# Kernel tuning notes

Hardware: AMD Instinct MI355X
Metric: run time of the kernel (lower is better)

The kernel has to match this reference:

```python
import jax, jax.numpy as jnp
import numpy as np

B_, L_, DIN, DM, DS, DR, K = 2, 1024, 1024, 2048, 16, 128, 4


def setup_inputs() -> dict:
    key = jax.random.key(0)
    ks = jax.random.split(key, 10)
    s = lambda k, shape, sc=0.02: (jax.random.normal(k, shape, jnp.float32) * sc)
    A_init = jnp.tile(jnp.arange(1, DS + 1, dtype=jnp.float32)[None, :], (DM, 1))  # (DM, DS)
    return {
        'x_in': jax.random.normal(ks[0], (B_, L_, DIN), jnp.float32),
        'W_in': s(ks[1], (DIN, DM)),
        'W_res': s(ks[2], (DIN, DM)),
        'W_out': s(ks[3], (DM, DIN)),
        'conv_w': s(ks[4], (DM, K), 0.1),   # depthwise conv weight (torch shape (DM,1,K) squeezed)
        'conv_b': jnp.zeros((DM,), jnp.float32),
        'A_log': jnp.log(A_init),
        'D': jnp.ones((DM,), jnp.float32),
        'W_B': s(ks[5], (DM, DS)),
        'W_C': s(ks[6], (DM, DS)),
        'W_dt': s(ks[7], (DM, DR)),
        'dt_w': s(ks[8], (DR, DM)),
        'dt_b': jnp.zeros((DM,), jnp.float32),
    }


def reference(x_in, W_in, W_res, W_out, conv_w, conv_b, A_log, D, W_B, W_C, W_dt, dt_w, dt_b):
    Bb, L, _ = x_in.shape
    x = x_in @ W_in                     # (B, L, DM)
    res = x_in @ W_res                  # (B, L, DM)
    # Causal depthwise conv1d: pad left k-1, truncate to L (matches Conv1d(padding=k-1)[:, :, :L])
    xp = jnp.pad(x, ((0, 0), (K - 1, 0), (0, 0)))
    xc = conv_b
    for i in range(K):
        xc = xc + xp[:, i:i + L, :] * conv_w[:, i]
    xc = jax.nn.silu(xc)                # (B, L, DM)
    # Selective SSM (fused_ssm)
    A = -jnp.exp(A_log)                 # (DM, DS)
    Bp = xc @ W_B                       # (B, L, DS)
    Cp = xc @ W_C                       # (B, L, DS)
    delta = jax.nn.softplus((xc @ W_dt) @ dt_w + dt_b)  # (B, L, DM)
    dA = jnp.exp(delta[..., None] * A)                       # (B, L, DM, DS)
    dBu = delta[..., None] * Bp[:, :, None, :] * xc[..., None]  # (B, L, DM, DS)

    def step(h, inp):
        dA_t, dBu_t, C_t = inp
        h = dA_t * h + dBu_t                         # (B, DM, DS)
        y = jnp.einsum('bdn,bn->bd', h, C_t)         # (B, DM)
        return h, y

    h0 = jnp.zeros((Bb, DM, DS), jnp.float32)
    _, ys = jax.lax.scan(step, h0, (dA.transpose(1, 0, 2, 3), dBu.transpose(1, 0, 2, 3), Cp.transpose(1, 0, 2)))
    y = ys.transpose(1, 0, 2) + D * xc  # (B, L, DM)
    y = y * jax.nn.silu(res)
    return y @ W_out                    # (B, L, DIN)
```

## Files before the change

kernel.cpp:

```cpp
#include <hip/hip_runtime.h>
#include <hip/hip_bf16.h>

constexpr int B_  = 2;
constexpr int L_  = 1024;
constexpr int DIN = 1024;
constexpr int DM  = 2048;
constexpr int DS  = 16;
constexpr int DR  = 128;
constexpr int KC  = 4;
constexpr int M_  = B_ * L_;
constexpr int NP2 = 256;
constexpr int KSLICES = 8;
constexpr int KSL = DM / KSLICES;
constexpr int OSLICES = 2;
constexpr int OSL = DM / OSLICES;

constexpr int NC = 32;
constexpr int CL = L_ / NC;
constexpr int S_ = B_ * DM * DS;

typedef __bf16 bf16x8 __attribute__((ext_vector_type(8)));
typedef float  f32x4  __attribute__((ext_vector_type(4)));

__device__ __forceinline__ void gload_lds16(const void* g, void* l) {
    __builtin_amdgcn_global_load_lds(
        (const __attribute__((address_space(1))) void*)g,
        (__attribute__((address_space(3))) void*)l, 16, 0, 0);
}

__device__ __forceinline__ void transpose_block(const float* __restrict__ in,
                                                __bf16* __restrict__ out,
                                                int R, int C, int bx, int by, int t) {
    __shared__ float tile[32][33];
    int tx = t & 31, ty = t >> 5;
    #pragma unroll
    for (int j = 0; j < 32; j += 8)
        tile[ty + j][tx] = in[(size_t)(by * 32 + ty + j) * C + (bx * 32 + tx)];
    __syncthreads();
    #pragma unroll
    for (int j = 0; j < 32; j += 8)
        out[(size_t)(bx * 32 + ty + j) * R + (by * 32 + tx)] = (__bf16)tile[tx][ty + j];
}

__global__ void prep_all(const float* __restrict__ x_in, const float* __restrict__ W_in,
                         const float* __restrict__ W_res, const float* __restrict__ W_out,
                         const float* __restrict__ dt_w,
                         const float* __restrict__ W_B, const float* __restrict__ W_C,
                         const float* __restrict__ W_dt,
                         __bf16* __restrict__ xinB, __bf16* __restrict__ WinT,
                         __bf16* __restrict__ WresT, __bf16* __restrict__ WoutT,
                         __bf16* __restrict__ dtwT, __bf16* __restrict__ projW) {
    int blk = blockIdx.x, t = threadIdx.x;
    if (blk < 8192) {
        int i = blk * 256 + t;
        xinB[i] = (__bf16)x_in[i];
    } else if (blk < 10240) {
        int b = blk - 8192;
        transpose_block(W_in, WinT, DIN, DM, b % 64, b / 64, t);
    } else if (blk < 12288) {
        int b = blk - 10240;
        transpose_block(W_res, WresT, DIN, DM, b % 64, b / 64, t);
    } else if (blk < 14336) {
        int b = blk - 12288;
        transpose_block(W_out, WoutT, DM, DIN, b % 32, b / 32, t);
    } else if (blk < 14592) {
        int b = blk - 14336;
        transpose_block(dt_w, dtwT, DR, DM, b % 64, b / 64, t);
    } else {
        int i = (blk - 14592) * 256 + t;
        int k = i % DM;
        int n = i / DM;
        float v = 0.f;
        if (n < 16)        v = W_B[(size_t)k * DS + n];
        else if (n < 32)   v = W_C[(size_t)k * DS + (n - 16)];
        else if (n < 160)  v = W_dt[(size_t)k * DR + (n - 32)];
        projW[i] = (__bf16)v;
    }
}

__global__ void reduce_split(const float* __restrict__ Ppart, float* __restrict__ Bp,
                             float* __restrict__ Cp, __bf16* __restrict__ dtmpB) {
    int i = blockIdx.x * 256 + threadIdx.x;
    int row = i / 160, c = i % 160;
    float v = 0.f;
    #pragma unroll
    for (int ks = 0; ks < KSLICES; ks++)
        v += Ppart[(size_t)ks * M_ * NP2 + (size_t)row * NP2 + c];
    if (c < 16)       Bp[(size_t)row * DS + c] = v;
    else if (c < 32)  Cp[(size_t)row * DS + (c - 16)] = v;
    else              dtmpB[(size_t)row * DR + (c - 32)] = (__bf16)v;
}

__global__ void reduce_out(const float* __restrict__ Opart, float* __restrict__ out) {
    int i = blockIdx.x * 256 + threadIdx.x;
    f32x4 s = ((const f32x4*)Opart)[i];
    #pragma unroll
    for (int ks = 1; ks < OSLICES; ks++)
        s += ((const f32x4*)(Opart + (size_t)ks * M_ * DIN))[i];
    ((f32x4*)out)[i] = s;
}

template<int EPI>
__global__ void gemm_tile128(const __bf16* __restrict__ A, const __bf16* __restrict__ BT,
                             float* __restrict__ Cf, __bf16* __restrict__ Cb,
                             const float* __restrict__ bias, int M, int N, int K,
                             int lda, int ldb) {
    __shared__ __bf16 sA[128 * 32];
    __shared__ __bf16 sB[128 * 32];
    int t = threadIdx.x;
    int lane = t & 63, w = t >> 6;
    int wm = w >> 1, wn = w & 1;
    int m0 = blockIdx.y * 128, n0 = blockIdx.x * 128;
    int kbase = blockIdx.z * K;
    int q = lane >> 4, rr = lane & 15;

    f32x4 acc[4][4] = {};

    int srow = t >> 2;
    int slot = t & 3;

    for (int kt = 0; kt < K; kt += 32) {
        __syncthreads();
        #pragma unroll
        for (int rnd = 0; rnd < 2; rnd++) {
            int row = srow + rnd * 64;
            int gkb = slot ^ ((row >> 1) & 3);
            const __bf16* ga = A  + (size_t)(m0 + row) * lda + kbase + kt + gkb * 8;
            const __bf16* gb = BT + (size_t)(n0 + row) * ldb + kbase + kt + gkb * 8;
            __bf16* la = sA + rnd * 2048 + w * 512;
            __bf16* lb = sB + rnd * 2048 + w * 512;
            gload_lds16(ga, la);
            gload_lds16(gb, lb);
        }
        __syncthreads();

        bf16x8 af[4], bfr[4];
        #pragma unroll
        for (int i = 0; i < 4; i++) {
            int rowA = wm * 64 + i * 16 + rr;
            af[i] = *(const bf16x8*)(sA + rowA * 32 + ((q ^ ((rowA >> 1) & 3)) * 8));
            int rowB = wn * 64 + i * 16 + rr;
            bfr[i] = *(const bf16x8*)(sB + rowB * 32 + ((q ^ ((rowB >> 1) & 3)) * 8));
        }
        #pragma unroll
        for (int i = 0; i < 4; i++)
            #pragma unroll
            for (int j = 0; j < 4; j++)
                acc[i][j] = __builtin_amdgcn_mfma_f32_16x16x32_bf16(af[i], bfr[j], acc[i][j], 0, 0, 0);
    }

    float* Cz = Cf + (size_t)blockIdx.z * M * N;
    #pragma unroll
    for (int i = 0; i < 4; i++) {
        #pragma unroll
        for (int j = 0; j < 4; j++) {
            int col = n0 + wn * 64 + j * 16 + rr;
            #pragma unroll
            for (int jj = 0; jj < 4; jj++) {
                int row = m0 + wm * 64 + i * 16 + q * 4 + jj;
                float v = acc[i][j][jj];
                if (EPI == 0) {
                    Cz[(size_t)row * N + col] = v;
                } else if (EPI == 1) {
                    float z = v + bias[col];
                    Cb[(size_t)row * N + col] = (__bf16)((z > 20.f) ? z : log1pf(__expf(z)));
                } else {
                    if (col < DM) ((__bf16*)Cf)[(size_t)row * DM + col] = (__bf16)v;
                    else          Cb[(size_t)row * DM + (col - DM)] = (__bf16)v;
                }
            }
        }
    }
}

__global__ void conv_silu(const __bf16* __restrict__ x, const float* __restrict__ w,
                          const float* __restrict__ bias, __bf16* __restrict__ xcB) {
    int idx = blockIdx.x * 256 + threadIdx.x;
    int d  = idx % DM;
    int bl = idx / DM;
    int l  = bl % L_;
    float acc = bias[d];
    #pragma unroll
    for (int i = 0; i < KC; i++) {
        int li = l - (KC - 1) + i;
        if (li >= 0) acc += (float)x[idx + (i - (KC - 1)) * DM] * w[d * KC + i];
    }
    float v = acc / (1.f + __expf(-acc));
    xcB[idx] = (__bf16)v;
}

__global__ void scan_phase1(const __bf16* __restrict__ delta, const __bf16* __restrict__ xc,
                            const float* __restrict__ Bp, const float* __restrict__ A_log,
                            float* __restrict__ aprod, float* __restrict__ cend) {
    int blk = blockIdx.x;
    int c   = blk % NC;
    int rem = blk / NC;
    int dmt = rem % (DM / 256);
    int b   = rem / (DM / 256);
    int t   = threadIdx.x;
    int dm  = dmt * 256 + t;
    int l0  = c * CL;

    __shared__ float sB[CL * DS];
    sB[t]       = Bp[((size_t)b * L_ + l0) * DS + t];
    sB[t + 256] = Bp[((size_t)b * L_ + l0) * DS + t + 256];
    __syncthreads();

    float Aval[DS];
    {
        const f32x4* Ap = (const f32x4*)(A_log + (size_t)dm * DS);
        #pragma unroll
        for (int r4 = 0; r4 < 4; r4++) {
            f32x4 a = Ap[r4];
            #pragma unroll
            for (int q = 0; q < 4; q++) Aval[r4 * 4 + q] = -__expf(a[q]);
        }
    }

    float h[DS], ap[DS];
    #pragma unroll
    for (int i = 0; i < DS; i++) { h[i] = 0.f; ap[i] = 1.f; }

    size_t base = ((size_t)b * L_ + l0) * DM + dm;
    #pragma unroll 4
    for (int j = 0; j < CL; j++) {
        float dl  = (float)delta[base + (size_t)j * DM];
        float xv  = (float)xc[base + (size_t)j * DM];
        float cmn = dl * xv;
        const f32x4* sB4 = (const f32x4*)(sB + j * DS);
        #pragma unroll
        for (int r4 = 0; r4 < 4; r4++) {
            f32x4 bv = sB4[r4];
            #pragma unroll
            for (int q = 0; q < 4; q++) {
                int i = r4 * 4 + q;
                float dA = __expf(dl * Aval[i]);
                ap[i] *= dA;
                h[i] = fmaf(dA, h[i], cmn * bv[q]);
            }
        }
    }

    size_t s = ((size_t)(b * DM + dm)) * DS;
    f32x4* apo = (f32x4*)(aprod + (size_t)c * S_ + s);
    f32x4* ceo = (f32x4*)(cend  + (size_t)c * S_ + s);
    #pragma unroll
    for (int r4 = 0; r4 < 4; r4++) {
        f32x4 va, vh;
        #pragma unroll
        for (int q = 0; q < 4; q++) { va[q] = ap[r4 * 4 + q]; vh[q] = h[r4 * 4 + q]; }
        apo[r4] = va; ceo[r4] = vh;
    }
}

__global__ void scan_phase2(const float* __restrict__ aprod, const float* __restrict__ cend,
                            float* __restrict__ hinit) {
    int u = blockIdx.x * 256 + threadIdx.x;
    float h = 0.f;
    #pragma unroll
    for (int c = 0; c < NC; c++) {
        hinit[(size_t)c * S_ + u] = h;
        h = fmaf(aprod[(size_t)c * S_ + u], h, cend[(size_t)c * S_ + u]);
    }
}

__global__ void scan_phase3(const __bf16* __restrict__ delta, const __bf16* __restrict__ xc,
                            const float* __restrict__ Bp, const float* __restrict__ Cp,
                            const __bf16* __restrict__ res, const float* __restrict__ A_log,
                            const float* __restrict__ Dw, const float* __restrict__ hinit,
                            __bf16* __restrict__ ybar) {
    int blk = blockIdx.x;
    int c   = blk % NC;
    int rem = blk / NC;
    int dmt = rem % (DM / 256);
    int b   = rem / (DM / 256);
    int t   = threadIdx.x;
    int dm  = dmt * 256 + t;
    int l0  = c * CL;

    __shared__ float sB[CL * DS];
    __shared__ float sC[CL * DS];
    sB[t]       = Bp[((size_t)b * L_ + l0) * DS + t];
    sB[t + 256] = Bp[((size_t)b * L_ + l0) * DS + t + 256];
    sC[t]       = Cp[((size_t)b * L_ + l0) * DS + t];
    sC[t + 256] = Cp[((size_t)b * L_ + l0) * DS + t + 256];
    __syncthreads();

    float Aval[DS];
    {
        const f32x4* Ap = (const f32x4*)(A_log + (size_t)dm * DS);
        #pragma unroll
        for (int r4 = 0; r4 < 4; r4++) {
            f32x4 a = Ap[r4];
            #pragma unroll
            for (int q = 0; q < 4; q++) Aval[r4 * 4 + q] = -__expf(a[q]);
        }
    }
    float Dval = Dw[dm];

    float h[DS];
    {
        const f32x4* hi = (const f32x4*)(hinit + (size_t)c * S_ + ((size_t)(b * DM + dm)) * DS);
        #pragma unroll
        for (int r4 = 0; r4 < 4; r4++) {
            f32x4 v = hi[r4];
            #pragma unroll
            for (int q = 0; q < 4; q++) h[r4 * 4 + q] = v[q];
        }
    }

    size_t base = ((size_t)b * L_ + l0) * DM + dm;
    #pragma unroll 4
    for (int j = 0; j < CL; j++) {
        float dl  = (float)delta[base + (size_t)j * DM];
        float xv  = (float)xc[base + (size_t)j * DM];
        float rv  = (float)res[base + (size_t)j * DM];
        float cmn = dl * xv;
        float y = 0.f;
        const f32x4* sB4 = (const f32x4*)(sB + j * DS);
        const f32x4* sC4 = (const f32x4*)(sC + j * DS);
        #pragma unroll
        for (int r4 = 0; r4 < 4; r4++) {
            f32x4 bv = sB4[r4];
            f32x4 cv = sC4[r4];
            #pragma unroll
            for (int q = 0; q < 4; q++) {
                int i = r4 * 4 + q;
                float dA = __expf(dl * Aval[i]);
                h[i] = fmaf(dA, h[i], cmn * bv[q]);
                y = fmaf(h[i], cv[q], y);
            }
        }
        float g = rv / (1.f + __expf(-rv));
        ybar[base + (size_t)j * DM] = (__bf16)((y + Dval * xv) * g);
    }
}

extern "C" void kernel_launch(void* const* d_in, const int* in_sizes, int n_in,
                              void* d_out, int out_size, void* d_ws, size_t ws_size,
                              hipStream_t stream) {
    const float* x_in   = (const float*)d_in[0];
    const float* W_in   = (const float*)d_in[1];
    const float* W_res  = (const float*)d_in[2];
    const float* W_out  = (const float*)d_in[3];
    const float* conv_w = (const float*)d_in[4];
    const float* conv_b = (const float*)d_in[5];
    const float* A_log  = (const float*)d_in[6];
    const float* Dw     = (const float*)d_in[7];
    const float* W_B    = (const float*)d_in[8];
    const float* W_C    = (const float*)d_in[9];
    const float* W_dt   = (const float*)d_in[10];
    const float* dt_w   = (const float*)d_in[11];
    const float* dt_b   = (const float*)d_in[12];

    float* ws_f = (float*)d_ws;
    float* Ppart = ws_f;
    float* Opart = Ppart + (size_t)KSLICES * M_ * NP2;
    float* Bp    = Opart + (size_t)OSLICES * M_ * DIN;
    float* Cp    = Bp    + (size_t)M_ * DS;
    float* aprod = Cp    + (size_t)M_ * DS;
    float* cend  = aprod + (size_t)NC * S_;
    float* hinit = cend  + (size_t)NC * S_;
    __bf16* bf_base = (__bf16*)(hinit + (size_t)NC * S_);
    __bf16* ybar   = bf_base;
    __bf16* xinB   = ybar   + (size_t)M_ * DM;
    __bf16* WinT   = xinB   + (size_t)M_ * DIN;
    __bf16* WresT  = WinT   + (size_t)DM * DIN;
    __bf16* WoutT  = WresT  + (size_t)DM * DIN;
    __bf16* xB     = WoutT  + (size_t)DIN * DM;
    __bf16* xcB    = xB     + (size_t)M_ * DM;
    __bf16* projW  = xcB    + (size_t)M_ * DM;
    __bf16* dtwT   = projW  + (size_t)NP2 * DM;
    __bf16* dtmpB  = dtwT   + (size_t)DM * DR;
    __bf16* deltaB = dtmpB  + (size_t)M_ * DR;
    __bf16* resB   = deltaB + (size_t)M_ * DM;

    prep_all<<<16640, 256, 0, stream>>>(x_in, W_in, W_res, W_out, dt_w, W_B, W_C, W_dt,
                                        xinB, WinT, WresT, WoutT, dtwT, projW);

    gemm_tile128<2><<<dim3((2 * DM) / 128, M_ / 128, 1), 256, 0, stream>>>(
        xinB, WinT, (float*)xB, resB, nullptr, M_, 2 * DM, DIN, DIN, DIN);

    conv_silu<<<(M_ * DM) / 256, 256, 0, stream>>>(xB, conv_w, conv_b, xcB);

    gemm_tile128<0><<<dim3(NP2 / 128, M_ / 128, KSLICES), 256, 0, stream>>>(
        xcB, projW, Ppart, nullptr, nullptr, M_, NP2, KSL, DM, DM);
    reduce_split<<<(M_ * 160) / 256, 256, 0, stream>>>(Ppart, Bp, Cp, dtmpB);

    gemm_tile128<1><<<dim3(DM / 128, M_ / 128, 1), 256, 0, stream>>>(
        dtmpB, dtwT, nullptr, deltaB, dt_b, M_, DM, DR, DR, DR);

    int nblk = B_ * (DM / 256) * NC;
    scan_phase1<<<nblk, 256, 0, stream>>>(deltaB, xcB, Bp, A_log, aprod, cend);
    scan_phase2<<<S_ / 256, 256, 0, stream>>>(aprod, cend, hinit);
    scan_phase3<<<nblk, 256, 0, stream>>>(deltaB, xcB, Bp, Cp, resB, A_log, Dw, hinit, ybar);

    gemm_tile128<0><<<dim3(DIN / 128, M_ / 128, OSLICES), 256, 0, stream>>>(
        ybar, WoutT, Opart, nullptr, nullptr, M_, DIN, OSL, DM, DM);
    reduce_out<<<(M_ * DIN) / 1024, 256, 0, stream>>>(Opart, (float*)d_out);
}
```

Baseline: 283.5 us.

## Vectorize conv, store scan carries in bf16, replace split-K output GEMM with 128x64 tile

Conv+SiLU now handles 8 channels per thread using a pretransposed tap-major conv weight. The chunked-scan carries (aprod, cend, hinit) are stored in bf16, and phase2 processes 8 states per thread. The split-K output GEMM and its reduction kernel are replaced by one 128x64-tile GEMM that writes the output directly. This cuts memory traffic and a launch, at the cost of bf16 precision on the scan carry state and fewer output blocks.

```diff
diff --git a/kernel.cpp b/kernel.cpp
--- a/kernel.cpp
+++ b/kernel.cpp
@@ -12,8 +12,6 @@
 constexpr int NP2 = 256;
 constexpr int KSLICES = 8;
 constexpr int KSL = DM / KSLICES;
-constexpr int OSLICES = 2;
-constexpr int OSL = DM / OSLICES;
 
 constexpr int NC = 32;
 constexpr int CL = L_ / NC;
@@ -46,10 +44,11 @@
                          const float* __restrict__ W_res, const float* __restrict__ W_out,
                          const float* __restrict__ dt_w,
                          const float* __restrict__ W_B, const float* __restrict__ W_C,
-                         const float* __restrict__ W_dt,
+                         const float* __restrict__ W_dt, const float* __restrict__ conv_w,
                          __bf16* __restrict__ xinB, __bf16* __restrict__ WinT,
                          __bf16* __restrict__ WresT, __bf16* __restrict__ WoutT,
-                         __bf16* __restrict__ dtwT, __bf16* __restrict__ projW) {
+                         __bf16* __restrict__ dtwT, __bf16* __restrict__ projW,
+                         float* __restrict__ cwT) {
     int blk = blockIdx.x, t = threadIdx.x;
     if (blk < 8192) {
         int i = blk * 256 + t;
@@ -66,7 +65,7 @@
     } else if (blk < 14592) {
         int b = blk - 14336;
         transpose_block(dt_w, dtwT, DR, DM, b % 64, b / 64, t);
-    } else {
+    } else if (blk < 16640) {
         int i = (blk - 14592) * 256 + t;
         int k = i % DM;
         int n = i / DM;
@@ -75,6 +74,10 @@
         else if (n < 32)   v = W_C[(size_t)k * DS + (n - 16)];
         else if (n < 160)  v = W_dt[(size_t)k * DR + (n - 32)];
         projW[i] = (__bf16)v;
+    } else {
+        int j = (blk - 16640) * 256 + t;
+        int tap = j / DM, d = j % DM;
+        cwT[j] = conv_w[d * KC + tap];
     }
 }
 
@@ -89,15 +92,6 @@
     if (c < 16)       Bp[(size_t)row * DS + c] = v;
     else if (c < 32)  Cp[(size_t)row * DS + (c - 16)] = v;
     else              dtmpB[(size_t)row * DR + (c - 32)] = (__bf16)v;
-}
-
-__global__ void reduce_out(const float* __restrict__ Opart, float* __restrict__ out) {
-    int i = blockIdx.x * 256 + threadIdx.x;
-    f32x4 s = ((const f32x4*)Opart)[i];
-    #pragma unroll
-    for (int ks = 1; ks < OSLICES; ks++)
-        s += ((const f32x4*)(Opart + (size_t)ks * M_ * DIN))[i];
-    ((f32x4*)out)[i] = s;
 }
 
 template<int EPI>
@@ -173,25 +167,110 @@
     }
 }
 
-__global__ void conv_silu(const __bf16* __restrict__ x, const float* __restrict__ w,
+__global__ void gemm_out64(const __bf16* __restrict__ A, const __bf16* __restrict__ BT,
+                           float* __restrict__ C, int M, int N, int K, int lda, int ldb) {
+    __shared__ __bf16 sA[128 * 32];
+    __shared__ __bf16 sB[64 * 32];
+    int t = threadIdx.x;
+    int lane = t & 63, w = t >> 6;
+    int m0 = blockIdx.y * 128, n0 = blockIdx.x * 64;
+    int q = lane >> 4, rr = lane & 15;
+
+    f32x4 acc[2][4] = {};
+    int srow = t >> 2;
+    int slot = t & 3;
+
+    for (int kt = 0; kt < K; kt += 32) {
+        __syncthreads();
+        #pragma unroll
+        for (int rnd = 0; rnd < 2; rnd++) {
+            int row = srow + rnd * 64;
+            int gkb = slot ^ ((row >> 1) & 3);
+            const __bf16* ga = A + (size_t)(m0 + row) * lda + kt + gkb * 8;
+            __bf16* la = sA + rnd * 2048 + w * 512;
+            gload_lds16(ga, la);
+        }
+        {
+            int row = srow;
+            int gkb = slot ^ ((row >> 1) & 3);
+            const __bf16* gb = BT + (size_t)(n0 + row) * ldb + kt + gkb * 8;
+            __bf16* lb = sB + w * 512;
+            gload_lds16(gb, lb);
+        }
+        __syncthreads();
+
+        bf16x8 af[2], bfr[4];
+        #pragma unroll
+        for (int i = 0; i < 2; i++) {
+            int rowA = w * 32 + i * 16 + rr;
+            af[i] = *(const bf16x8*)(sA + rowA * 32 + ((q ^ ((rowA >> 1) & 3)) * 8));
+        }
+        #pragma unroll
+        for (int j = 0; j < 4; j++) {
+            int rowB = j * 16 + rr;
+            bfr[j] = *(const bf16x8*)(sB + rowB * 32 + ((q ^ ((rowB >> 1) & 3)) * 8));
+        }
+        #pragma unroll
+        for (int i = 0; i < 2; i++)
+            #pragma unroll
+            for (int j = 0; j < 4; j++)
+                acc[i][j] = __builtin_amdgcn_mfma_f32_16x16x32_bf16(af[i], bfr[j], acc[i][j], 0, 0, 0);
+    }
+
+    #pragma unroll
+    for (int i = 0; i < 2; i++) {
+        #pragma unroll
+        for (int j = 0; j < 4; j++) {
+            int col = n0 + j * 16 + rr;
+            #pragma unroll
+            for (int jj = 0; jj < 4; jj++) {
+                int row = m0 + w * 32 + i * 16 + q * 4 + jj;
+                C[(size_t)row * N + col] = acc[i][j][jj];
+            }
+        }
+    }
+}
+
+__global__ void conv_silu(const __bf16* __restrict__ x, const float* __restrict__ cwT,
                           const float* __restrict__ bias, __bf16* __restrict__ xcB) {
-    int idx = blockIdx.x * 256 + threadIdx.x;
-    int d  = idx % DM;
-    int bl = idx / DM;
-    int l  = bl % L_;
-    float acc = bias[d];
+    int row = blockIdx.x;
+    int d   = threadIdx.x * 8;
+    int l   = row % L_;
+    size_t base = (size_t)row * DM + d;
+
+    float acc[8];
+    {
+        const f32x4* b4 = (const f32x4*)(bias + d);
+        f32x4 b0 = b4[0], b1 = b4[1];
+        #pragma unroll
+        for (int q = 0; q < 4; q++) { acc[q] = b0[q]; acc[4 + q] = b1[q]; }
+    }
     #pragma unroll
     for (int i = 0; i < KC; i++) {
         int li = l - (KC - 1) + i;
-        if (li >= 0) acc += (float)x[idx + (i - (KC - 1)) * DM] * w[d * KC + i];
-    }
-    float v = acc / (1.f + __expf(-acc));
-    xcB[idx] = (__bf16)v;
+        if (li >= 0) {
+            bf16x8 xv = *(const bf16x8*)(x + base + (size_t)(i - (KC - 1)) * DM);
+            const f32x4* w4 = (const f32x4*)(cwT + (size_t)i * DM + d);
+            f32x4 w0 = w4[0], w1 = w4[1];
+            #pragma unroll
+            for (int q = 0; q < 4; q++) {
+                acc[q]     = fmaf((float)xv[q],     w0[q], acc[q]);
+                acc[4 + q] = fmaf((float)xv[4 + q], w1[q], acc[4 + q]);
+            }
+        }
+    }
+    bf16x8 out;
+    #pragma unroll
+    for (int q = 0; q < 8; q++) {
+        float v = acc[q] / (1.f + __expf(-acc[q]));
+        out[q] = (__bf16)v;
+    }
+    *(bf16x8*)(xcB + base) = out;
 }
 
 __global__ void scan_phase1(const __bf16* __restrict__ delta, const __bf16* __restrict__ xc,
                             const float* __restrict__ Bp, const float* __restrict__ A_log,
-                            float* __restrict__ aprod, float* __restrict__ cend) {
+                            __bf16* __restrict__ aprodB, __bf16* __restrict__ cendB) {
     int blk = blockIdx.x;
     int c   = blk % NC;
     int rem = blk / NC;
@@ -242,32 +321,40 @@
     }
 
     size_t s = ((size_t)(b * DM + dm)) * DS;
-    f32x4* apo = (f32x4*)(aprod + (size_t)c * S_ + s);
-    f32x4* ceo = (f32x4*)(cend  + (size_t)c * S_ + s);
-    #pragma unroll
-    for (int r4 = 0; r4 < 4; r4++) {
-        f32x4 va, vh;
-        #pragma unroll
-        for (int q = 0; q < 4; q++) { va[q] = ap[r4 * 4 + q]; vh[q] = h[r4 * 4 + q]; }
-        apo[r4] = va; ceo[r4] = vh;
-    }
-}
-
-__global__ void scan_phase2(const float* __restrict__ aprod, const float* __restrict__ cend,
-                            float* __restrict__ hinit) {
-    int u = blockIdx.x * 256 + threadIdx.x;
-    float h = 0.f;
+    #pragma unroll
+    for (int r8 = 0; r8 < 2; r8++) {
+        bf16x8 va, vh;
+        #pragma unroll
+        for (int q = 0; q < 8; q++) { va[q] = (__bf16)ap[r8 * 8 + q]; vh[q] = (__bf16)h[r8 * 8 + q]; }
+        ((bf16x8*)(aprodB + (size_t)c * S_ + s))[r8] = va;
+        ((bf16x8*)(cendB  + (size_t)c * S_ + s))[r8] = vh;
+    }
+}
+
+__global__ void scan_phase2(const __bf16* __restrict__ aprodB, const __bf16* __restrict__ cendB,
+                            __bf16* __restrict__ hinitB) {
+    int u8 = (blockIdx.x * 256 + threadIdx.x) * 8;
+    float h[8];
+    #pragma unroll
+    for (int q = 0; q < 8; q++) h[q] = 0.f;
     #pragma unroll
     for (int c = 0; c < NC; c++) {
-        hinit[(size_t)c * S_ + u] = h;
-        h = fmaf(aprod[(size_t)c * S_ + u], h, cend[(size_t)c * S_ + u]);
+        bf16x8 a = *(const bf16x8*)(aprodB + (size_t)c * S_ + u8);
+        bf16x8 ce = *(const bf16x8*)(cendB + (size_t)c * S_ + u8);
+        bf16x8 ho;
+        #pragma unroll
+        for (int q = 0; q < 8; q++) {
+            ho[q] = (__bf16)h[q];
+            h[q] = fmaf((float)a[q], h[q], (float)ce[q]);
+        }
+        *(bf16x8*)(hinitB + (size_t)c * S_ + u8) = ho;
     }
 }
 
 __global__ void scan_phase3(const __bf16* __restrict__ delta, const __bf16* __restrict__ xc,
                             const float* __restrict__ Bp, const float* __restrict__ Cp,
                             const __bf16* __restrict__ res, const float* __restrict__ A_log,
-                            const float* __restrict__ Dw, const float* __restrict__ hinit,
+                            const float* __restrict__ Dw, const __bf16* __restrict__ hinitB,
                             __bf16* __restrict__ ybar) {
     int blk = blockIdx.x;
     int c   = blk % NC;
@@ -300,12 +387,12 @@
 
     float h[DS];
     {
-        const f32x4* hi = (const f32x4*)(hinit + (size_t)c * S_ + ((size_t)(b * DM + dm)) * DS);
-        #pragma unroll
-        for (int r4 = 0; r4 < 4; r4++) {
-            f32x4 v = hi[r4];
-            #pragma unroll
-            for (int q = 0; q < 4; q++) h[r4 * 4 + q] = v[q];
+        size_t s = ((size_t)(b * DM + dm)) * DS;
+        #pragma unroll
+        for (int r8 = 0; r8 < 2; r8++) {
+            bf16x8 v = ((const bf16x8*)(hinitB + (size_t)c * S_ + s))[r8];
+            #pragma unroll
+            for (int q = 0; q < 8; q++) h[r8 * 8 + q] = (float)v[q];
         }
     }
 
@@ -355,13 +442,10 @@
 
     float* ws_f = (float*)d_ws;
     float* Ppart = ws_f;
-    float* Opart = Ppart + (size_t)KSLICES * M_ * NP2;
-    float* Bp    = Opart + (size_t)OSLICES * M_ * DIN;
+    float* Bp    = Ppart + (size_t)KSLICES * M_ * NP2;
     float* Cp    = Bp    + (size_t)M_ * DS;
-    float* aprod = Cp    + (size_t)M_ * DS;
-    float* cend  = aprod + (size_t)NC * S_;
-    float* hinit = cend  + (size_t)NC * S_;
-    __bf16* bf_base = (__bf16*)(hinit + (size_t)NC * S_);
+    float* cwT   = Cp    + (size_t)M_ * DS;
+    __bf16* bf_base = (__bf16*)(cwT + (size_t)KC * DM);
     __bf16* ybar   = bf_base;
     __bf16* xinB   = ybar   + (size_t)M_ * DM;
     __bf16* WinT   = xinB   + (size_t)M_ * DIN;
@@ -374,14 +458,17 @@
     __bf16* dtmpB  = dtwT   + (size_t)DM * DR;
     __bf16* deltaB = dtmpB  + (size_t)M_ * DR;
     __bf16* resB   = deltaB + (size_t)M_ * DM;
-
-    prep_all<<<16640, 256, 0, stream>>>(x_in, W_in, W_res, W_out, dt_w, W_B, W_C, W_dt,
-                                        xinB, WinT, WresT, WoutT, dtwT, projW);
+    __bf16* aprodB = resB   + (size_t)M_ * DM;
+    __bf16* cendB  = aprodB + (size_t)NC * S_;
+    __bf16* hinitB = cendB  + (size_t)NC * S_;
+
+    prep_all<<<16672, 256, 0, stream>>>(x_in, W_in, W_res, W_out, dt_w, W_B, W_C, W_dt,
+                                        conv_w, xinB, WinT, WresT, WoutT, dtwT, projW, cwT);
 
     gemm_tile128<2><<<dim3((2 * DM) / 128, M_ / 128, 1), 256, 0, stream>>>(
         xinB, WinT, (float*)xB, resB, nullptr, M_, 2 * DM, DIN, DIN, DIN);
 
-    conv_silu<<<(M_ * DM) / 256, 256, 0, stream>>>(xB, conv_w, conv_b, xcB);
+    conv_silu<<<M_, 256, 0, stream>>>(xB, cwT, conv_b, xcB);
 
     gemm_tile128<0><<<dim3(NP2 / 128, M_ / 128, KSLICES), 256, 0, stream>>>(
         xcB, projW, Ppart, nullptr, nullptr, M_, NP2, KSL, DM, DM);
@@ -391,11 +478,10 @@
         dtmpB, dtwT, nullptr, deltaB, dt_b, M_, DM, DR, DR, DR);
 
     int nblk = B_ * (DM / 256) * NC;
-    scan_phase1<<<nblk, 256, 0, stream>>>(deltaB, xcB, Bp, A_log, aprod, cend);
-    scan_phase2<<<S_ / 256, 256, 0, stream>>>(aprod, cend, hinit);
-    scan_phase3<<<nblk, 256, 0, stream>>>(deltaB, xcB, Bp, Cp, resB, A_log, Dw, hinit, ybar);
-
-    gemm_tile128<0><<<dim3(DIN / 128, M_ / 128, OSLICES), 256, 0, stream>>>(
-        ybar, WoutT, Opart, nullptr, nullptr, M_, DIN, OSL, DM, DM);
-    reduce_out<<<(M_ * DIN) / 1024, 256, 0, stream>>>(Opart, (float*)d_out);
-}
+    scan_phase1<<<nblk, 256, 0, stream>>>(deltaB, xcB, Bp, A_log, aprodB, cendB);
+    scan_phase2<<<S_ / (256 * 8), 256, 0, stream>>>(aprodB, cendB, hinitB);
+    scan_phase3<<<nblk, 256, 0, stream>>>(deltaB, xcB, Bp, Cp, resB, A_log, Dw, hinitB, ybar);
+
+    gemm_out64<<<dim3(DIN / 64, M_ / 128), 256, 0, stream>>>(
+        ybar, WoutT, (float*)d_out, M_, DIN, DM, DM, DM);
+}
```

Measured after the change: 267.1 us. -5.8%, faster.
